# Kernel optimization log

Measured on AMD Instinct MI355X. Metric: run time of the kernel, lower is better.

## Reference

```python
import jax, jax.numpy as jnp
import numpy as np

NUM_HEADS = 16

def rotate_half(x):
    x1, x2 = jnp.split(x, 2, axis=-1)
    return jnp.concatenate([-x2, x1], axis=-1)

def setup_inputs() -> dict:
    key = jax.random.key(0)
    ks = jax.random.split(key, 12)
    B, S, D = 2, 2048, 1024
    sc = 1.0 / np.sqrt(D)
    return {
        "x": jax.random.normal(ks[0], (B, S, D), dtype=jnp.float32),
        "cdr_mask": jax.random.uniform(ks[1], (B, 1, S, S), dtype=jnp.float32),
        "Wq": jax.random.normal(ks[2], (D, D), dtype=jnp.float32) * sc,
        "bq": jnp.zeros((D,), dtype=jnp.float32),
        "Wk": jax.random.normal(ks[3], (D, D), dtype=jnp.float32) * sc,
        "bk": jnp.zeros((D,), dtype=jnp.float32),
        "Wv": jax.random.normal(ks[4], (D, D), dtype=jnp.float32) * sc,
        "bv": jnp.zeros((D,), dtype=jnp.float32),
        "Wo": jax.random.normal(ks[5], (D, D), dtype=jnp.float32) * sc,
        "bo": jnp.zeros((D,), dtype=jnp.float32),
        "cdr_weight": jnp.asarray(1.0, dtype=jnp.float32),
    }

def reference(x, cdr_mask, Wq, bq, Wk, bk, Wv, bv, Wo, bo, cdr_weight):
    B, S, D = x.shape
    H = NUM_HEADS
    hd = D // H
    # RoPE tables: NOTE original uses full head_dim frequencies (not head_dim/2)
    inv_freq = 1.0 / (10000.0 ** (jnp.arange(hd, dtype=jnp.float32) / hd))
    pos = jnp.arange(S, dtype=jnp.float32)
    sinusoid = pos[:, None] * inv_freq[None, :]          # [S, hd]
    sin_pos = jnp.sin(sinusoid)[None, None]              # [1,1,S,hd]
    cos_pos = jnp.cos(sinusoid)[None, None]

    def heads(y):  # [B,S,D] -> [B,H,S,hd]
        return y.reshape(B, S, H, hd).transpose(0, 2, 1, 3)

    Q = heads(x @ Wq + bq)
    K = heads(x @ Wk + bk)
    V = heads(x @ Wv + bv)
    Qr = Q * cos_pos + rotate_half(Q) * sin_pos
    Kr = K * cos_pos + rotate_half(K) * sin_pos

    scores = jnp.einsum('bhqd,bhkd->bhqk', Qr, Kr) / jnp.sqrt(jnp.asarray(hd, x.dtype))
    scores = scores * (1.0 + cdr_mask * cdr_weight)      # multiplicative learned mask
    attn = jax.nn.softmax(scores, axis=-1)               # dropout is identity in eval
    out = jnp.einsum('bhqk,bhkd->bhqd', attn, V)
    out = out.transpose(0, 2, 1, 3).reshape(B, S, D)
    return out @ Wo + bo
```

## Files before the change

### kernel.cpp

```cpp
#include <hip/hip_runtime.h>
#include <stdint.h>

typedef unsigned short u16;
typedef __bf16 bf16x8 __attribute__((ext_vector_type(8)));
typedef float f32x4 __attribute__((ext_vector_type(4)));
typedef float fx4 __attribute__((ext_vector_type(4)));
typedef unsigned short u16x8 __attribute__((ext_vector_type(8)));
typedef unsigned short u16x4 __attribute__((ext_vector_type(4)));

#define DEV __device__ __forceinline__

DEV u16 f2bf(float f) {
  unsigned u = __builtin_bit_cast(unsigned, f);
  u += 0x7fff + ((u >> 16) & 1);
  return (u16)(u >> 16);
}

DEV f32x4 mfma16(bf16x8 a, bf16x8 b, f32x4 c) {
  return __builtin_amdgcn_mfma_f32_16x16x32_bf16(a, b, c, 0, 0, 0);
}

DEV void gload16(const void* g, void* l) {
  __builtin_amdgcn_global_load_lds(
      (const __attribute__((address_space(1))) unsigned int*)g,
      (__attribute__((address_space(3))) unsigned int*)l, 16, 0, 0);
}

__global__ __launch_bounds__(256) void k_tables(float* __restrict__ cosT,
                                                float* __restrict__ sinT) {
  int i = blockIdx.x * 256 + threadIdx.x;
  int s = i >> 6, d = i & 63;
  float inv = exp2f(-(float)d * (13.287712379549449f / 64.f));
  float a = (float)s * inv;
  cosT[i] = cosf(a);
  sinT[i] = sinf(a);
}

__global__ __launch_bounds__(256) void k_cvt(const float* __restrict__ x,
                                             u16* __restrict__ xb) {
  int i = (blockIdx.x * 256 + threadIdx.x) * 4;
  fx4 f = *reinterpret_cast<const fx4*>(x + i);
  u16x4 o;
#pragma unroll
  for (int j = 0; j < 4; ++j) o[j] = f2bf(f[j]);
  *reinterpret_cast<u16x4*>(xb + i) = o;
}

__global__ __launch_bounds__(256) void k_wtrans(
    const float* __restrict__ W0, const float* __restrict__ W1,
    const float* __restrict__ W2, const float* __restrict__ W3,
    u16* __restrict__ O0, u16* __restrict__ O1,
    u16* __restrict__ O2, u16* __restrict__ O3) {
  __shared__ u16 T[64][66];
  const float* W = (blockIdx.z == 0) ? W0 : (blockIdx.z == 1) ? W1
                   : (blockIdx.z == 2) ? W2 : W3;
  u16* O = (blockIdx.z == 0) ? O0 : (blockIdx.z == 1) ? O1
           : (blockIdx.z == 2) ? O2 : O3;
  const int t = threadIdx.x;
  const int k0 = blockIdx.y * 64, n0 = blockIdx.x * 64;
  const int r = t >> 2, cc = (t & 3) * 16;
  const float* src = W + (long)(k0 + r) * 1024 + n0 + cc;
#pragma unroll
  for (int u = 0; u < 16; u += 4) {
    fx4 f = *reinterpret_cast<const fx4*>(src + u);
#pragma unroll
    for (int j = 0; j < 4; ++j) T[r][cc + u + j] = f2bf(f[j]);
  }
  __syncthreads();
  const int n = t >> 2, kc = (t & 3) * 16;
  u16x8 o1, o2;
#pragma unroll
  for (int j = 0; j < 8; ++j) { o1[j] = T[kc + j][n]; o2[j] = T[kc + 8 + j][n]; }
  u16* dst = O + (long)(n0 + n) * 1024 + k0 + kc;
  *reinterpret_cast<u16x8*>(dst) = o1;
  *reinterpret_cast<u16x8*>(dst + 8) = o2;
}

__global__ __launch_bounds__(256) void k_gemm_qkv(
    const u16* __restrict__ A, const u16* __restrict__ Bt,
    const float* __restrict__ bq, const float* __restrict__ bk,
    const float* __restrict__ bv, const float* __restrict__ cosT,
    const float* __restrict__ sinT, u16* __restrict__ qb,
    u16* __restrict__ kb, u16* __restrict__ vb) {
  __shared__ u16 As[128 * 32];
  __shared__ u16 Bs[128 * 32];
  const int t = threadIdx.x;
  const int lane = t & 63, wid = t >> 6;
  const int wm = wid >> 1, wn = wid & 1;
  const int l15 = lane & 15, lg = lane >> 4;
  const int bm = blockIdx.x, bn = blockIdx.y;

  f32x4 acc[4][4];
#pragma unroll
  for (int m = 0; m < 4; ++m)
#pragma unroll
    for (int n = 0; n < 4; ++n) acc[m][n] = f32x4{0.f, 0.f, 0.f, 0.f};

  const int arow = t >> 2;
  const int acol = (t & 3) << 3;
  const u16* Ab = A + (long)(bm * 128 + arow) * 1024 + acol;
  const u16* Bb = Bt + (long)(bn * 128 + arow) * 1024 + acol;

  for (int k0 = 0; k0 < 1024; k0 += 32) {
    gload16(Ab + k0, As + t * 8);
    gload16(Ab + 64 * 1024 + k0, As + 2048 + t * 8);
    gload16(Bb + k0, Bs + t * 8);
    gload16(Bb + 64 * 1024 + k0, Bs + 2048 + t * 8);
    __syncthreads();
    bf16x8 af[4], bfr[4];
#pragma unroll
    for (int m = 0; m < 4; ++m)
      af[m] = *reinterpret_cast<const bf16x8*>(As + (wm * 64 + m * 16 + l15) * 32 + lg * 8);
#pragma unroll
    for (int n = 0; n < 4; ++n)
      bfr[n] = *reinterpret_cast<const bf16x8*>(Bs + (wn * 64 + n * 16 + l15) * 32 + lg * 8);
#pragma unroll
    for (int m = 0; m < 4; ++m)
#pragma unroll
      for (int n = 0; n < 4; ++n) acc[m][n] = mfma16(af[m], bfr[n], acc[m][n]);
    __syncthreads();
  }

  const int seg = bn >> 3;
  const float* bias = (seg == 0) ? bq : (seg == 1) ? bk : bv;
  u16* outb = (seg == 0) ? qb : (seg == 1) ? kb : vb;
  const int h = (bn & 7) * 2 + wn;
#pragma unroll
  for (int m = 0; m < 4; ++m) {
#pragma unroll
    for (int reg = 0; reg < 4; ++reg) {
      const int rg = bm * 128 + wm * 64 + m * 16 + lg * 4 + reg;
      const int s = rg & 2047, b = rg >> 11;
      float v4[4];
#pragma unroll
      for (int n = 0; n < 4; ++n)
        v4[n] = acc[m][n][reg] + bias[(bn & 7) * 128 + wn * 64 + n * 16 + l15];
      if (seg < 2) {
#pragma unroll
        for (int n = 0; n < 4; ++n) {
          const int d = n * 16 + l15;
          float c = cosT[s * 64 + d], sn = sinT[s * 64 + d];
          float rot = (n < 2) ? -v4[n + 2] : v4[n - 2];
          outb[((long)(b * 16 + h) * 2048 + s) * 64 + d] = f2bf(v4[n] * c + rot * sn);
        }
      } else {
#pragma unroll
        for (int n = 0; n < 4; ++n)
          outb[((long)(b * 16 + h) * 2048 + s) * 64 + n * 16 + l15] = f2bf(v4[n]);
      }
    }
  }
}

__global__ __launch_bounds__(256) void k_gemm_out(
    const u16* __restrict__ A, const u16* __restrict__ Bt,
    const float* __restrict__ bias, float* __restrict__ outf) {
  __shared__ u16 As[128 * 32];
  __shared__ u16 Bs[128 * 32];
  const int t = threadIdx.x;
  const int lane = t & 63, wid = t >> 6;
  const int wm = wid >> 1, wn = wid & 1;
  const int l15 = lane & 15, lg = lane >> 4;
  const int bm = blockIdx.x, bn = blockIdx.y;

  f32x4 acc[4][4];
#pragma unroll
  for (int m = 0; m < 4; ++m)
#pragma unroll
    for (int n = 0; n < 4; ++n) acc[m][n] = f32x4{0.f, 0.f, 0.f, 0.f};

  const int arow = t >> 2;
  const int acol = (t & 3) << 3;
  const u16* Ab = A + (long)(bm * 128 + arow) * 1024 + acol;
  const u16* Bb = Bt + (long)(bn * 128 + arow) * 1024 + acol;

  for (int k0 = 0; k0 < 1024; k0 += 32) {
    gload16(Ab + k0, As + t * 8);
    gload16(Ab + 64 * 1024 + k0, As + 2048 + t * 8);
    gload16(Bb + k0, Bs + t * 8);
    gload16(Bb + 64 * 1024 + k0, Bs + 2048 + t * 8);
    __syncthreads();
    bf16x8 af[4], bfr[4];
#pragma unroll
    for (int m = 0; m < 4; ++m)
      af[m] = *reinterpret_cast<const bf16x8*>(As + (wm * 64 + m * 16 + l15) * 32 + lg * 8);
#pragma unroll
    for (int n = 0; n < 4; ++n)
      bfr[n] = *reinterpret_cast<const bf16x8*>(Bs + (wn * 64 + n * 16 + l15) * 32 + lg * 8);
#pragma unroll
    for (int m = 0; m < 4; ++m)
#pragma unroll
      for (int n = 0; n < 4; ++n) acc[m][n] = mfma16(af[m], bfr[n], acc[m][n]);
    __syncthreads();
  }

#pragma unroll
  for (int m = 0; m < 4; ++m)
#pragma unroll
    for (int reg = 0; reg < 4; ++reg) {
      const int rg = bm * 128 + wm * 64 + m * 16 + lg * 4 + reg;
#pragma unroll
      for (int n = 0; n < 4; ++n)
        outf[(long)rg * 1024 + bn * 128 + wn * 64 + n * 16 + l15] =
            acc[m][n][reg] + bias[bn * 128 + wn * 64 + n * 16 + l15];
    }
}

__global__ __launch_bounds__(256) void k_vtrans(const u16* __restrict__ VB,
                                                u16* __restrict__ VT) {
  __shared__ u16 T[64][66];
  const int t = threadIdx.x;
  const int bh = blockIdx.y;
  const int s0 = blockIdx.x * 64;
  const int r = t >> 2, c = (t & 3) * 16;
  const u16* src = VB + ((long)bh * 2048 + s0 + r) * 64 + c;
  u16x8 a = *reinterpret_cast<const u16x8*>(src);
  u16x8 b = *reinterpret_cast<const u16x8*>(src + 8);
#pragma unroll
  for (int j = 0; j < 8; ++j) { T[r][c + j] = a[j]; T[r][c + 8 + j] = b[j]; }
  __syncthreads();
  const int d = t >> 2, sc = (t & 3) * 16;
  u16x8 o1, o2;
#pragma unroll
  for (int j = 0; j < 8; ++j) { o1[j] = T[sc + j][d]; o2[j] = T[sc + 8 + j][d]; }
  u16* dst = VT + ((long)bh * 64 + d) * 2048 + s0 + sc;
  *reinterpret_cast<u16x8*>(dst) = o1;
  *reinterpret_cast<u16x8*>(dst + 8) = o2;
}

__global__ __launch_bounds__(256, 4) void k_attn(
    const u16* __restrict__ Qb, const u16* __restrict__ Kb,
    const u16* __restrict__ Vt, const float* __restrict__ mask,
    const float* __restrict__ wp, u16* __restrict__ Ob) {
  __shared__ u16 Ks[2][64 * 64];
  __shared__ u16 Vs[2][64 * 64];
  __shared__ u16 Ps[4][16 * 64];
  const int t = threadIdx.x, lane = t & 63, wid = t >> 6;
  const int l15 = lane & 15, lg = lane >> 4;
  const int b = blockIdx.z, hh = blockIdx.y;
  const int bh = b * 16 + hh;
  const int qw = blockIdx.x * 64 + wid * 16;
  const float c1 = 0.18033688f;
  const float c2 = c1 * wp[0];

  bf16x8 qf[2];
  const u16* Qrow = Qb + ((long)bh * 2048 + qw + l15) * 64 + lg * 8;
  qf[0] = *reinterpret_cast<const bf16x8*>(Qrow);
  qf[1] = *reinterpret_cast<const bf16x8*>(Qrow + 32);

  bf16x8 ones;
#pragma unroll
  for (int j = 0; j < 8; ++j) ones[j] = (__bf16)1.0f;

  f32x4 oacc[4];
#pragma unroll
  for (int n = 0; n < 4; ++n) oacc[n] = f32x4{0.f, 0.f, 0.f, 0.f};
  f32x4 lsum = f32x4{0.f, 0.f, 0.f, 0.f};

  const u16* Kbase = Kb + (long)bh * 2048 * 64;
  const u16* Vbase = Vt + (long)bh * 64 * 2048;
  const float* Mbase = mask + (long)b * 2048 * 2048 + (long)(qw + lg * 4) * 2048 + l15;

  const int krow = t >> 3;
  const int kcs = ((t & 7) * 8) ^ ((krow & 7) << 3);

#define STAGE(buf, kt)                                                       \
  do {                                                                       \
    gload16(Kbase + (long)((kt) + krow) * 64 + kcs, Ks[buf] + t * 8);        \
    gload16(Kbase + (long)((kt) + krow + 32) * 64 + kcs,                     \
            Ks[buf] + 2048 + t * 8);                                         \
    gload16(Vbase + (long)krow * 2048 + (kt) + kcs, Vs[buf] + t * 8);        \
    gload16(Vbase + (long)(krow + 32) * 2048 + (kt) + kcs,                   \
            Vs[buf] + 2048 + t * 8);                                         \
  } while (0)

  STAGE(0, 0);
  __syncthreads();
  int cur = 0;

  for (int kt = 0; kt < 2048; kt += 64) {
    if (kt + 64 < 2048) STAGE(cur ^ 1, kt + 64);

    float mv[4][4];
#pragma unroll
    for (int reg = 0; reg < 4; ++reg)
#pragma unroll
      for (int n = 0; n < 4; ++n)
        mv[reg][n] = Mbase[(long)reg * 2048 + kt + n * 16];

    f32x4 sc[4];
#pragma unroll
    for (int n = 0; n < 4; ++n) sc[n] = f32x4{0.f, 0.f, 0.f, 0.f};
#pragma unroll
    for (int ks = 0; ks < 2; ++ks) {
      const int ko = (ks * 32 + lg * 8) ^ ((l15 & 7) << 3);
#pragma unroll
      for (int n = 0; n < 4; ++n) {
        bf16x8 kf = *reinterpret_cast<const bf16x8*>(Ks[cur] + (n * 16 + l15) * 64 + ko);
        sc[n] = mfma16(qf[ks], kf, sc[n]);
      }
    }

#pragma unroll
    for (int n = 0; n < 4; ++n)
#pragma unroll
      for (int reg = 0; reg < 4; ++reg) {
        float mult = __builtin_fmaf(mv[reg][n], c2, c1);
        float p = __builtin_amdgcn_exp2f(sc[n][reg] * mult);
        const int r = lg * 4 + reg;
        Ps[wid][r * 64 + ((n * 16 + l15) ^ ((r & 7) << 3))] =
            __builtin_bit_cast(u16, (__bf16)p);
      }

#pragma unroll
    for (int ks = 0; ks < 2; ++ks) {
      const int ko = (ks * 32 + lg * 8) ^ ((l15 & 7) << 3);
      bf16x8 pf = *reinterpret_cast<const bf16x8*>(Ps[wid] + l15 * 64 + ko);
      lsum = mfma16(pf, ones, lsum);
#pragma unroll
      for (int n = 0; n < 4; ++n) {
        bf16x8 vf = *reinterpret_cast<const bf16x8*>(Vs[cur] + (n * 16 + l15) * 64 + ko);
        oacc[n] = mfma16(pf, vf, oacc[n]);
      }
    }
    __syncthreads();
    cur ^= 1;
  }
#undef STAGE

#pragma unroll
  for (int n = 0; n < 4; ++n)
#pragma unroll
    for (int reg = 0; reg < 4; ++reg) {
      float v = oacc[n][reg] / lsum[reg];
      Ob[((long)b * 2048 + qw + lg * 4 + reg) * 1024 + hh * 64 + n * 16 + l15] = f2bf(v);
    }
}

extern "C" void kernel_launch(void* const* d_in, const int* in_sizes, int n_in,
                              void* d_out, int out_size, void* d_ws, size_t ws_size,
                              hipStream_t stream) {
  const float* x  = (const float*)d_in[0];
  const float* cm = (const float*)d_in[1];
  const float* Wq = (const float*)d_in[2];
  const float* bq = (const float*)d_in[3];
  const float* Wk = (const float*)d_in[4];
  const float* bk = (const float*)d_in[5];
  const float* Wv = (const float*)d_in[6];
  const float* bv = (const float*)d_in[7];
  const float* Wo = (const float*)d_in[8];
  const float* bo = (const float*)d_in[9];
  const float* cw = (const float*)d_in[10];
  float* out = (float*)d_out;

  char* ws = (char*)d_ws;
  float* cosT = (float*)(ws + 0);
  float* sinT = (float*)(ws + (512u << 10));
  u16* xb  = (u16*)(ws + (1u << 20));
  u16* wqT = (u16*)(ws + (9u << 20));
  u16* woT = (u16*)(ws + (15u << 20));
  u16* qb  = (u16*)(ws + (17u << 20));
  u16* kb  = (u16*)(ws + (25u << 20));
  u16* vb  = (u16*)(ws + (33u << 20));
  u16* vt  = (u16*)(ws + (41u << 20));
  u16* ob  = (u16*)(ws + (49u << 20));
  u16* wkT = wqT + (1u << 20);
  u16* wvT = wqT + (2u << 20);

  k_tables<<<512, 256, 0, stream>>>(cosT, sinT);
  k_cvt<<<4096, 256, 0, stream>>>(x, xb);
  k_wtrans<<<dim3(16, 16, 4), 256, 0, stream>>>(Wq, Wk, Wv, Wo, wqT, wkT, wvT, woT);
  k_gemm_qkv<<<dim3(32, 24), 256, 0, stream>>>(xb, wqT, bq, bk, bv, cosT, sinT, qb, kb, vb);
  k_vtrans<<<dim3(32, 32), 256, 0, stream>>>(vb, vt);
  k_attn<<<dim3(32, 16, 2), 256, 0, stream>>>(qb, kb, vt, cm, cw, ob);
  k_gemm_out<<<dim3(32, 8), 256, 0, stream>>>(ob, woT, bo, out);
}
```

Baseline: 251.5 us.

## Keep softmax probabilities in registers via transposed QK MFMA and lane permutes

The QK^T MFMA operands are swapped so each lane holds scores for one query row across keys. The exp results are packed to bf16 and rearranged into the PV MFMA A-operand layout with permlane32/permlane16 swaps. This removes the per-wave LDS scratch for P and its store/load round trip. The mask is now read as contiguous float4 per lane instead of scattered scalar loads. The cost is an explicit round-to-nearest bf16 conversion and the cross-lane permutes, and the kernel depends on the permlane swap builtins being available on this target.

```diff
diff --git a/kernel.cpp b/kernel.cpp
--- a/kernel.cpp
+++ b/kernel.cpp
@@ -2,11 +2,14 @@
 #include <stdint.h>
 
 typedef unsigned short u16;
+typedef unsigned u32;
 typedef __bf16 bf16x8 __attribute__((ext_vector_type(8)));
 typedef float f32x4 __attribute__((ext_vector_type(4)));
 typedef float fx4 __attribute__((ext_vector_type(4)));
 typedef unsigned short u16x8 __attribute__((ext_vector_type(8)));
 typedef unsigned short u16x4 __attribute__((ext_vector_type(4)));
+typedef unsigned u32x2 __attribute__((ext_vector_type(2)));
+typedef unsigned u32x4 __attribute__((ext_vector_type(4)));
 
 #define DEV __device__ __forceinline__
 
@@ -14,6 +17,10 @@
   unsigned u = __builtin_bit_cast(unsigned, f);
   u += 0x7fff + ((u >> 16) & 1);
   return (u16)(u >> 16);
+}
+
+DEV u32 pk2(float a, float b) {
+  return (u32)f2bf(a) | ((u32)f2bf(b) << 16);
 }
 
 DEV f32x4 mfma16(bf16x8 a, bf16x8 b, f32x4 c) {
@@ -234,7 +241,6 @@
     const float* __restrict__ wp, u16* __restrict__ Ob) {
   __shared__ u16 Ks[2][64 * 64];
   __shared__ u16 Vs[2][64 * 64];
-  __shared__ u16 Ps[4][16 * 64];
   const int t = threadIdx.x, lane = t & 63, wid = t >> 6;
   const int l15 = lane & 15, lg = lane >> 4;
   const int b = blockIdx.z, hh = blockIdx.y;
@@ -259,7 +265,7 @@
 
   const u16* Kbase = Kb + (long)bh * 2048 * 64;
   const u16* Vbase = Vt + (long)bh * 64 * 2048;
-  const float* Mbase = mask + (long)b * 2048 * 2048 + (long)(qw + lg * 4) * 2048 + l15;
+  const float* Mrow = mask + (long)b * 2048 * 2048 + (long)(qw + l15) * 2048 + 4 * lg;
 
   const int krow = t >> 3;
   const int kcs = ((t & 7) * 8) ^ ((krow & 7) << 3);
@@ -281,13 +287,6 @@
   for (int kt = 0; kt < 2048; kt += 64) {
     if (kt + 64 < 2048) STAGE(cur ^ 1, kt + 64);
 
-    float mv[4][4];
-#pragma unroll
-    for (int reg = 0; reg < 4; ++reg)
-#pragma unroll
-      for (int n = 0; n < 4; ++n)
-        mv[reg][n] = Mbase[(long)reg * 2048 + kt + n * 16];
-
     f32x4 sc[4];
 #pragma unroll
     for (int n = 0; n < 4; ++n) sc[n] = f32x4{0.f, 0.f, 0.f, 0.f};
@@ -297,30 +296,43 @@
 #pragma unroll
       for (int n = 0; n < 4; ++n) {
         bf16x8 kf = *reinterpret_cast<const bf16x8*>(Ks[cur] + (n * 16 + l15) * 64 + ko);
-        sc[n] = mfma16(qf[ks], kf, sc[n]);
+        sc[n] = mfma16(kf, qf[ks], sc[n]);
       }
     }
 
-#pragma unroll
-    for (int n = 0; n < 4; ++n)
-#pragma unroll
-      for (int reg = 0; reg < 4; ++reg) {
-        float mult = __builtin_fmaf(mv[reg][n], c2, c1);
-        float p = __builtin_amdgcn_exp2f(sc[n][reg] * mult);
-        const int r = lg * 4 + reg;
-        Ps[wid][r * 64 + ((n * 16 + l15) ^ ((r & 7) << 3))] =
-            __builtin_bit_cast(u16, (__bf16)p);
-      }
+    float p[4][4];
+#pragma unroll
+    for (int n = 0; n < 4; ++n) {
+      fx4 mv = *reinterpret_cast<const fx4*>(Mrow + kt + 16 * n);
+#pragma unroll
+      for (int reg = 0; reg < 4; ++reg)
+        p[n][reg] = __builtin_amdgcn_exp2f(sc[n][reg] *
+                                           __builtin_fmaf(mv[reg], c2, c1));
+    }
+
+    bf16x8 pf[2];
+#pragma unroll
+    for (int ks = 0; ks < 2; ++ks) {
+      u32 A0 = pk2(p[2 * ks][0], p[2 * ks][1]);
+      u32 A1 = pk2(p[2 * ks][2], p[2 * ks][3]);
+      u32 B0 = pk2(p[2 * ks + 1][0], p[2 * ks + 1][1]);
+      u32 B1 = pk2(p[2 * ks + 1][2], p[2 * ks + 1][3]);
+      u32x2 r0 = __builtin_amdgcn_permlane32_swap(A0, B0, false, false);
+      u32x2 r1 = __builtin_amdgcn_permlane32_swap(A1, B1, false, false);
+      u32x2 s0 = __builtin_amdgcn_permlane16_swap(r0[0], r0[1], false, false);
+      u32x2 s1 = __builtin_amdgcn_permlane16_swap(r1[0], r1[1], false, false);
+      u32x4 pw = {s0[0], s1[0], s0[1], s1[1]};
+      pf[ks] = __builtin_bit_cast(bf16x8, pw);
+    }
 
 #pragma unroll
     for (int ks = 0; ks < 2; ++ks) {
       const int ko = (ks * 32 + lg * 8) ^ ((l15 & 7) << 3);
-      bf16x8 pf = *reinterpret_cast<const bf16x8*>(Ps[wid] + l15 * 64 + ko);
-      lsum = mfma16(pf, ones, lsum);
+      lsum = mfma16(pf[ks], ones, lsum);
 #pragma unroll
       for (int n = 0; n < 4; ++n) {
         bf16x8 vf = *reinterpret_cast<const bf16x8*>(Vs[cur] + (n * 16 + l15) * 64 + ko);
-        oacc[n] = mfma16(pf, vf, oacc[n]);
+        oacc[n] = mfma16(pf[ks], vf, oacc[n]);
       }
     }
     __syncthreads();
```

Measured after the change: 260.7 us. 3.7% more time.
